# Kernel tuning notes

Hardware: AMD Instinct MI355X
Metric: run time of the kernel (lower is better)

The kernel has to match this reference:

```python
import jax, jax.numpy as jnp
import numpy as np

HIDDEN = 1024
HEADS = 16
HEAD = HIDDEN // HEADS
B, S = 2, 2048


def setup_inputs() -> dict:
    key = jax.random.key(0)
    ks = jax.random.split(key, 8)
    query = jax.random.normal(ks[0], (B, S, HIDDEN), dtype=jnp.float32)
    key_t = jax.random.normal(ks[1], (B, S, HIDDEN), dtype=jnp.float32)
    value = jax.random.normal(ks[2], (B, S, HIDDEN), dtype=jnp.float32)
    # causal mask, broadcastable over batch and heads; 0 -> masked (-inf)
    mask = jnp.tril(jnp.ones((S, S), dtype=jnp.int32))[None, None, :, :]
    # torch Linear weights are [out_features, in_features]
    scale = 0.02
    Wq = jax.random.normal(ks[3], (HIDDEN, HIDDEN), dtype=jnp.float32) * scale
    Wk = jax.random.normal(ks[4], (HIDDEN, HIDDEN), dtype=jnp.float32) * scale
    Wv = jax.random.normal(ks[5], (HIDDEN, HIDDEN), dtype=jnp.float32) * scale
    Wo = jax.random.normal(ks[6], (HIDDEN, HIDDEN), dtype=jnp.float32) * scale
    bo = jax.random.normal(ks[7], (HIDDEN,), dtype=jnp.float32) * scale
    return {"query": query, "key": key_t, "value": value, "mask": mask,
            "Wq": Wq, "Wk": Wk, "Wv": Wv, "Wo": Wo, "bo": bo}


def reference(query, key, value, mask, Wq, Wk, Wv, Wo, bo):
    b = query.shape[0]
    # Linear (no bias): x @ W^T, then split into heads -> [b, h, s, d]
    def heads(x, W):
        y = jnp.einsum('bse,oe->bso', x, W)
        return y.reshape(b, -1, HEADS, HEAD).transpose(0, 2, 1, 3)
    Q = heads(query, Wq)
    K = heads(key, Wk)
    V = heads(value, Wv)
    inv_scale = 1.0 / jnp.sqrt(jnp.float32(HEAD))
    scores = jnp.einsum('bhqd,bhkd->bhqk', Q, K) * inv_scale  # [b,h,s,s]
    scores = jnp.where(mask == 0, -jnp.inf, scores)
    attn = jax.nn.softmax(scores, axis=-1)
    x = jnp.einsum('bhqk,bhkd->bhqd', attn, V)
    x = x.transpose(0, 2, 1, 3).reshape(b, -1, HIDDEN)
    return jnp.einsum('bse,oe->bso', x, Wo) + bo
```

## Files before the change

kernel.cpp:

```cpp
#include <hip/hip_runtime.h>


typedef __attribute__((ext_vector_type(8))) short short8;
typedef __attribute__((ext_vector_type(4))) float f32x4;
typedef unsigned int u32;
typedef unsigned short u16;

__device__ inline f32x4 mfma16(short8 a, short8 b, f32x4 c) {
    return __builtin_amdgcn_mfma_f32_16x16x32_bf16(a, b, c, 0, 0, 0);
}
__device__ inline u16 f2bf(float f) {
    union { float f; u32 u; } v; v.f = f;
    u32 r = v.u + 0x7fff + ((v.u >> 16) & 1);
    return (u16)(r >> 16);
}
__device__ inline void gll16(void* lds, const void* g) {
    __builtin_amdgcn_global_load_lds((const __attribute__((address_space(1))) u32*)g,
                                     (__attribute__((address_space(3))) u32*)lds,
                                     16, 0, 0);
}
__device__ inline u32 pkbf(float hi, float lo) {
    return __builtin_amdgcn_perm(__float_as_uint(hi), __float_as_uint(lo),
                                 0x07060302u);
}

__global__ __launch_bounds__(256)
void cvt_all(const float* __restrict__ q, const float* __restrict__ k,
             const float* __restrict__ v, const float* __restrict__ wq,
             const float* __restrict__ wk, const float* __restrict__ wv,
             const float* __restrict__ wo,
             u16* __restrict__ q16, u16* __restrict__ k16,
             u16* __restrict__ v16, u16* __restrict__ w16) {
    const size_t QKV = 1u << 22;
    const size_t WSZ = 1u << 20;
    size_t base = ((size_t)blockIdx.x * 256 + threadIdx.x) * 8;
    const float* src; u16* dst; size_t off; float scale = 1.0f;
    if (base < QKV)            { src = q; dst = q16; off = base;
                                 scale = 0.125f * 1.44269504f; }
    else if (base < 2 * QKV)   { src = k; dst = k16; off = base - QKV;     }
    else if (base < 3 * QKV)   { src = v; dst = v16; off = base - 2 * QKV; }
    else {
        size_t wb = base - 3 * QKV;
        int wi = (int)(wb >> 20); off = wb & (WSZ - 1);
        src = wi == 0 ? wq : wi == 1 ? wk : wi == 2 ? wv : wo;
        dst = w16 + (size_t)wi * WSZ;
    }
    float4 f0 = *(const float4*)(src + off);
    float4 f1 = *(const float4*)(src + off + 4);
    short8 s = { (short)f2bf(f0.x * scale), (short)f2bf(f0.y * scale),
                 (short)f2bf(f0.z * scale), (short)f2bf(f0.w * scale),
                 (short)f2bf(f1.x * scale), (short)f2bf(f1.y * scale),
                 (short)f2bf(f1.z * scale), (short)f2bf(f1.w * scale) };
    *(short8*)(dst + off) = s;
}

__global__ __launch_bounds__(256)
void gemm_qkv(const u16* __restrict__ q16, const u16* __restrict__ k16,
              const u16* __restrict__ v16, const u16* __restrict__ w16,
              u16* __restrict__ Qg, u16* __restrict__ Kg, u16* __restrict__ Vt) {
    const int K = 1024;
    __shared__ u16 As[2][128 * 64];
    __shared__ u16 Bs[2][128 * 64];
    const int z = blockIdx.z;
    const u16* A = z == 0 ? q16 : z == 1 ? k16 : v16;
    const u16* W = w16 + (size_t)z * (1u << 20);

    const int tid = threadIdx.x, lane = tid & 63, w = tid >> 6;
    const int ln15 = lane & 15, quad = lane >> 4, s7 = ln15 & 7;
    const int lr = lane >> 3;
    const int lcs = (((lane & 7) ^ lr) << 3);
    const int m0 = blockIdx.y * 128, n0 = blockIdx.x * 128;
    const int wm = (w >> 1) * 64, wn = (w & 1) * 64;

    f32x4 acc[4][4] = {};

    #pragma unroll
    for (int c = 0; c < 4; ++c) {
        gll16(&As[0][(w * 32 + c * 8) * 64],
              &A[(size_t)(m0 + w * 32 + c * 8 + lr) * K + lcs]);
        gll16(&Bs[0][(w * 32 + c * 8) * 64],
              &W[(size_t)(n0 + w * 32 + c * 8 + lr) * K + lcs]);
    }

    for (int i = 0; i < 16; ++i) {
        const int cur = i & 1;
        if (i < 15) {
            const int nb = cur ^ 1, k0 = (i + 1) * 64;
            #pragma unroll
            for (int c = 0; c < 4; ++c) {
                gll16(&As[nb][(w * 32 + c * 8) * 64],
                      &A[(size_t)(m0 + w * 32 + c * 8 + lr) * K + k0 + lcs]);
                gll16(&Bs[nb][(w * 32 + c * 8) * 64],
                      &W[(size_t)(n0 + w * 32 + c * 8 + lr) * K + k0 + lcs]);
            }
            __asm__ volatile("s_waitcnt vmcnt(8)" ::: "memory");
        } else {
            __asm__ volatile("s_waitcnt vmcnt(0)" ::: "memory");
        }
        __builtin_amdgcn_s_barrier();

        #pragma unroll
        for (int kh = 0; kh < 2; ++kh) {
            short8 a[4], b[4];
            #pragma unroll
            for (int mt = 0; mt < 4; ++mt)
                a[mt] = *(const short8*)&As[cur][(wm + mt * 16 + ln15) * 64 +
                                                (((kh * 4 + quad) ^ s7) << 3)];
            #pragma unroll
            for (int nt = 0; nt < 4; ++nt)
                b[nt] = *(const short8*)&Bs[cur][(wn + nt * 16 + ln15) * 64 +
                                                (((kh * 4 + quad) ^ s7) << 3)];
            #pragma unroll
            for (int mt = 0; mt < 4; ++mt)
                #pragma unroll
                for (int nt = 0; nt < 4; ++nt)
                    acc[mt][nt] = mfma16(a[mt], b[nt], acc[mt][nt]);
        }
        __builtin_amdgcn_s_barrier();
    }

    #pragma unroll
    for (int mt = 0; mt < 4; ++mt)
        #pragma unroll
        for (int nt = 0; nt < 4; ++nt)
            #pragma unroll
            for (int r = 0; r < 4; ++r) {
                int m = m0 + wm + mt * 16 + quad * 4 + r;
                int n = n0 + wn + nt * 16 + ln15;
                u16 hv = f2bf(acc[mt][nt][r]);
                if (z == 2) {
                    int b_ = m >> 11, s_ = m & 2047, h_ = n >> 6, d_ = n & 63;
                    int kl = s_ & 63;
                    int sp = (s_ & ~63) + (kl & 15) * 4 + (kl >> 4);
                    Vt[((size_t)(b_ * 16 + h_) * 64 + d_) * 2048 + sp] = hv;
                } else {
                    u16* dst = z ? Kg : Qg;
                    dst[(size_t)m * 1024 + n] = hv;
                }
            }
}

__global__ __launch_bounds__(256)
void gemm_out(const u16* __restrict__ A, const u16* __restrict__ W,
              const float* __restrict__ bias, float* __restrict__ out) {
    const int K = 1024;
    __shared__ u16 As[2][64 * 64];
    __shared__ u16 Bs[2][128 * 64];
    const int id = blockIdx.x;
    const int by = id >> 3, bx = id & 7;

    const int tid = threadIdx.x, lane = tid & 63, w = tid >> 6;
    const int ln15 = lane & 15, quad = lane >> 4, s7 = ln15 & 7;
    const int lr = lane >> 3;
    const int lcs = (((lane & 7) ^ lr) << 3);
    const int m0 = by * 64, n0 = bx * 128;
    const int wm = (w & 1) * 32, wn = (w >> 1) * 64;

    f32x4 acc[2][4] = {};

    #pragma unroll
    for (int c = 0; c < 2; ++c)
        gll16(&As[0][(w * 16 + c * 8) * 64],
              &A[(size_t)(m0 + w * 16 + c * 8 + lr) * K + lcs]);
    #pragma unroll
    for (int c = 0; c < 4; ++c)
        gll16(&Bs[0][(w * 32 + c * 8) * 64],
              &W[(size_t)(n0 + w * 32 + c * 8 + lr) * K + lcs]);

    for (int i = 0; i < 16; ++i) {
        const int cur = i & 1;
        if (i < 15) {
            const int nb = cur ^ 1, k0 = (i + 1) * 64;
            #pragma unroll
            for (int c = 0; c < 2; ++c)
                gll16(&As[nb][(w * 16 + c * 8) * 64],
                      &A[(size_t)(m0 + w * 16 + c * 8 + lr) * K + k0 + lcs]);
            #pragma unroll
            for (int c = 0; c < 4; ++c)
                gll16(&Bs[nb][(w * 32 + c * 8) * 64],
                      &W[(size_t)(n0 + w * 32 + c * 8 + lr) * K + k0 + lcs]);
            __asm__ volatile("s_waitcnt vmcnt(6)" ::: "memory");
        } else {
            __asm__ volatile("s_waitcnt vmcnt(0)" ::: "memory");
        }
        __builtin_amdgcn_s_barrier();

        #pragma unroll
        for (int kh = 0; kh < 2; ++kh) {
            short8 a[2], b[4];
            #pragma unroll
            for (int mt = 0; mt < 2; ++mt)
                a[mt] = *(const short8*)&As[cur][(wm + mt * 16 + ln15) * 64 +
                                                (((kh * 4 + quad) ^ s7) << 3)];
            #pragma unroll
            for (int nt = 0; nt < 4; ++nt)
                b[nt] = *(const short8*)&Bs[cur][(wn + nt * 16 + ln15) * 64 +
                                                (((kh * 4 + quad) ^ s7) << 3)];
            #pragma unroll
            for (int mt = 0; mt < 2; ++mt)
                #pragma unroll
                for (int nt = 0; nt < 4; ++nt)
                    acc[mt][nt] = mfma16(a[mt], b[nt], acc[mt][nt]);
        }
        __builtin_amdgcn_s_barrier();
    }

    #pragma unroll
    for (int mt = 0; mt < 2; ++mt)
        #pragma unroll
        for (int nt = 0; nt < 4; ++nt)
            #pragma unroll
            for (int r = 0; r < 4; ++r) {
                int m = m0 + wm + mt * 16 + quad * 4 + r;
                int n = n0 + wn + nt * 16 + ln15;
                out[(size_t)m * 1024 + n] = acc[mt][nt][r] + bias[n];
            }
}

__global__ __launch_bounds__(256)
void attn3(const u16* __restrict__ Qg, const u16* __restrict__ Kg,
           const u16* __restrict__ Vt, u16* __restrict__ Xb) {
    __shared__ u16 Kl[2][64 * 64];
    __shared__ u16 Vl[2][64 * 64];
    __shared__ u16 Pl[4][16 * 72];

    const int id = blockIdx.x;
    const int bh = id & 31, qt = 31 - (id >> 5);
    const int b = bh >> 4, h = bh & 15;
    const int tid = threadIdx.x, lane = tid & 63, w = tid >> 6;
    const int ln15 = lane & 15, quad = lane >> 4, s7 = ln15 & 7;
    const int lr = lane >> 3;
    const int lcs = (((lane & 7) ^ lr) << 3);
    const u16* Kbase = Kg + (size_t)b * 2048 * 1024 + h * 64;
    const u16* Vbase = Vt + (size_t)bh * 64 * 2048;
    const float M0L = 8.65617025f;
    const int q0 = qt * 64;

    const u16* qrow = Qg + (size_t)(b * 2048 + q0 + w * 16 + ln15) * 1024 + h * 64;
    short8 aq0 = *(const short8*)(qrow + quad * 8);
    short8 aq1 = *(const short8*)(qrow + 32 + quad * 8);
    __asm__ volatile("s_waitcnt vmcnt(0)" ::: "memory");

    f32x4 o[4] = {};
    float lsum[4] = {0.f, 0.f, 0.f, 0.f};

    #pragma unroll
    for (int c = 0; c < 2; ++c) {
        const int r0 = w * 16 + c * 8;
        gll16(&Kl[0][r0 * 64], Kbase + (size_t)(r0 + lr) * 1024 + lcs);
        gll16(&Vl[0][r0 * 64], Vbase + (size_t)(r0 + lr) * 2048 + lcs);
    }

    for (int kt = 0; kt <= qt; ++kt) {
        const int cur = kt & 1;
        if (kt < qt) {
            const int nb = cur ^ 1, nk = (kt + 1) * 64;
            #pragma unroll
            for (int c = 0; c < 2; ++c) {
                const int r0 = w * 16 + c * 8;
                gll16(&Kl[nb][r0 * 64], Kbase + (size_t)(nk + r0 + lr) * 1024 + lcs);
                gll16(&Vl[nb][r0 * 64], Vbase + (size_t)(r0 + lr) * 2048 + nk + lcs);
            }
            __asm__ volatile("s_waitcnt vmcnt(4)" ::: "memory");
        } else {
            __asm__ volatile("s_waitcnt vmcnt(0)" ::: "memory");
        }
        __builtin_amdgcn_s_barrier();

        f32x4 sc[4];
        #pragma unroll
        for (int ct = 0; ct < 4; ++ct) {
            short8 b0 = *(const short8*)&Kl[cur][(ct * 16 + ln15) * 64 +
                                                ((quad ^ s7) << 3)];
            short8 b1 = *(const short8*)&Kl[cur][(ct * 16 + ln15) * 64 +
                                                (((4 + quad) ^ s7) << 3)];
            f32x4 c = {};
            c = mfma16(aq0, b0, c);
            c = mfma16(aq1, b1, c);
            sc[ct] = c;
        }

        const bool diag = (kt == qt);
        #pragma unroll
        for (int r = 0; r < 4; ++r) {
            float s0 = sc[0][r], s1 = sc[1][r], s2 = sc[2][r], s3 = sc[3][r];
            if (diag) {
                const int qq = w * 16 + quad * 4 + r;
                s0 = (ln15      <= qq) ? s0 : -1e30f;
                s1 = (16 + ln15 <= qq) ? s1 : -1e30f;
                s2 = (32 + ln15 <= qq) ? s2 : -1e30f;
                s3 = (48 + ln15 <= qq) ? s3 : -1e30f;
            }
            float p0 = __builtin_amdgcn_exp2f(s0 - M0L);
            float p1 = __builtin_amdgcn_exp2f(s1 - M0L);
            float p2 = __builtin_amdgcn_exp2f(s2 - M0L);
            float p3 = __builtin_amdgcn_exp2f(s3 - M0L);
            uint2 pw = make_uint2(pkbf(p1, p0), pkbf(p3, p2));
            *(uint2*)&Pl[w][(quad * 4 + r) * 72 + ln15 * 4] = pw;
            lsum[r] += (p0 + p1) + (p2 + p3);
        }

        __asm__ volatile("s_waitcnt lgkmcnt(0)" ::: "memory");
        short8 ap0 = *(const short8*)&Pl[w][ln15 * 72 + quad * 8];
        short8 ap1 = *(const short8*)&Pl[w][ln15 * 72 + 32 + quad * 8];

        #pragma unroll
        for (int dt = 0; dt < 4; ++dt) {
            short8 bv0 = *(const short8*)&Vl[cur][(dt * 16 + ln15) * 64 +
                                                 ((quad ^ s7) << 3)];
            short8 bv1 = *(const short8*)&Vl[cur][(dt * 16 + ln15) * 64 +
                                                 (((4 + quad) ^ s7) << 3)];
            o[dt] = mfma16(ap0, bv0, o[dt]);
            o[dt] = mfma16(ap1, bv1, o[dt]);
        }
        __builtin_amdgcn_s_barrier();
    }

    #pragma unroll
    for (int r = 0; r < 4; ++r) {
        float l = lsum[r];
        #pragma unroll
        for (int off = 1; off < 16; off <<= 1)
            l += __shfl_xor(l, off);
        lsum[r] = l;
    }
    #pragma unroll
    for (int dt = 0; dt < 4; ++dt)
        #pragma unroll
        for (int r = 0; r < 4; ++r) {
            int q = q0 + w * 16 + quad * 4 + r;
            Xb[(size_t)(b * 2048 + q) * 1024 + h * 64 + dt * 16 + ln15] =
                f2bf(o[dt][r] / lsum[r]);
        }
}

extern "C" void kernel_launch(void* const* d_in, const int* in_sizes, int n_in,
                              void* d_out, int out_size, void* d_ws, size_t ws_size,
                              hipStream_t stream) {
    const float* query = (const float*)d_in[0];
    const float* key   = (const float*)d_in[1];
    const float* value = (const float*)d_in[2];
    const float* Wq = (const float*)d_in[4];
    const float* Wk = (const float*)d_in[5];
    const float* Wv = (const float*)d_in[6];
    const float* Wo = (const float*)d_in[7];
    const float* bo = (const float*)d_in[8];
    float* out = (float*)d_out;

    u16* ws  = (u16*)d_ws;
    const size_t T = 1ull << 22;
    u16* q16 = ws;
    u16* k16 = ws + T;
    u16* v16 = ws + 2 * T;
    u16* w16 = ws + 3 * T;
    u16* Qg  = ws + 4 * T;
    u16* Kg  = ws + 5 * T;
    u16* Vt  = (u16*)d_out;
    u16* Xb  = q16;
    const size_t WSZ = 1ull << 20;

    cvt_all<<<8192, 256, 0, stream>>>(query, key, value, Wq, Wk, Wv, Wo,
                                      q16, k16, v16, w16);

    gemm_qkv<<<dim3(8, 32, 3), 256, 0, stream>>>(q16, k16, v16, w16, Qg, Kg, Vt);

    attn3<<<1024, 256, 0, stream>>>(Qg, Kg, Vt, Xb);

    gemm_out<<<512, 256, 0, stream>>>(Xb, w16 + 3 * WSZ, bo, out);
}
```

Baseline: 228.4 us.

## Enlarge QKV GEMM tiles to 256x256 with 512 threads and split B-tile prefetch

```diff
diff --git a/kernel.cpp b/kernel.cpp
--- a/kernel.cpp
+++ b/kernel.cpp
@@ -54,13 +54,13 @@
     *(short8*)(dst + off) = s;
 }
 
-__global__ __launch_bounds__(256)
+__global__ __launch_bounds__(512, 2)
 void gemm_qkv(const u16* __restrict__ q16, const u16* __restrict__ k16,
               const u16* __restrict__ v16, const u16* __restrict__ w16,
               u16* __restrict__ Qg, u16* __restrict__ Kg, u16* __restrict__ Vt) {
     const int K = 1024;
-    __shared__ u16 As[2][128 * 64];
-    __shared__ u16 Bs[2][128 * 64];
+    __shared__ u16 As[2][256 * 64];
+    __shared__ u16 Bs[2][256 * 64];
     const int z = blockIdx.z;
     const u16* A = z == 0 ? q16 : z == 1 ? k16 : v16;
     const u16* W = w16 + (size_t)z * (1u << 20);
@@ -69,58 +69,86 @@
     const int ln15 = lane & 15, quad = lane >> 4, s7 = ln15 & 7;
     const int lr = lane >> 3;
     const int lcs = (((lane & 7) ^ lr) << 3);
-    const int m0 = blockIdx.y * 128, n0 = blockIdx.x * 128;
-    const int wm = (w >> 1) * 64, wn = (w & 1) * 64;
-
-    f32x4 acc[4][4] = {};
-
-    #pragma unroll
-    for (int c = 0; c < 4; ++c) {
+    const int m0 = blockIdx.y * 256, n0 = blockIdx.x * 256;
+    const int wm = (w >> 2) * 128, wn = (w & 3) * 64;
+
+    f32x4 acc[8][4] = {};
+
+    #pragma unroll
+    for (int c = 0; c < 4; ++c)
         gll16(&As[0][(w * 32 + c * 8) * 64],
               &A[(size_t)(m0 + w * 32 + c * 8 + lr) * K + lcs]);
+    #pragma unroll
+    for (int c = 0; c < 4; ++c)
         gll16(&Bs[0][(w * 32 + c * 8) * 64],
               &W[(size_t)(n0 + w * 32 + c * 8 + lr) * K + lcs]);
-    }
-
-    for (int i = 0; i < 16; ++i) {
-        const int cur = i & 1;
-        if (i < 15) {
-            const int nb = cur ^ 1, k0 = (i + 1) * 64;
-            #pragma unroll
-            for (int c = 0; c < 4; ++c) {
+
+    for (int t = 0; t < 16; ++t) {
+        const int cur = t & 1, nb = cur ^ 1;
+        const int k0 = (t + 1) * 64;
+        if (t < 15) {
+            #pragma unroll
+            for (int c = 0; c < 4; ++c)
                 gll16(&As[nb][(w * 32 + c * 8) * 64],
                       &A[(size_t)(m0 + w * 32 + c * 8 + lr) * K + k0 + lcs]);
-                gll16(&Bs[nb][(w * 32 + c * 8) * 64],
-                      &W[(size_t)(n0 + w * 32 + c * 8 + lr) * K + k0 + lcs]);
-            }
-            __asm__ volatile("s_waitcnt vmcnt(8)" ::: "memory");
+            __asm__ volatile("s_waitcnt vmcnt(4)" ::: "memory");
         } else {
             __asm__ volatile("s_waitcnt vmcnt(0)" ::: "memory");
         }
         __builtin_amdgcn_s_barrier();
-
-        #pragma unroll
-        for (int kh = 0; kh < 2; ++kh) {
-            short8 a[4], b[4];
-            #pragma unroll
-            for (int mt = 0; mt < 4; ++mt)
+        __builtin_amdgcn_sched_barrier(0);
+
+        {
+            short8 a[8], b[4];
+            #pragma unroll
+            for (int mt = 0; mt < 8; ++mt)
                 a[mt] = *(const short8*)&As[cur][(wm + mt * 16 + ln15) * 64 +
-                                                (((kh * 4 + quad) ^ s7) << 3)];
+                                                ((quad ^ s7) << 3)];
             #pragma unroll
             for (int nt = 0; nt < 4; ++nt)
                 b[nt] = *(const short8*)&Bs[cur][(wn + nt * 16 + ln15) * 64 +
-                                                (((kh * 4 + quad) ^ s7) << 3)];
-            #pragma unroll
-            for (int mt = 0; mt < 4; ++mt)
+                                                ((quad ^ s7) << 3)];
+            __builtin_amdgcn_s_setprio(1);
+            #pragma unroll
+            for (int mt = 0; mt < 8; ++mt)
                 #pragma unroll
                 for (int nt = 0; nt < 4; ++nt)
                     acc[mt][nt] = mfma16(a[mt], b[nt], acc[mt][nt]);
-        }
-        __builtin_amdgcn_s_barrier();
-    }
-
-    #pragma unroll
-    for (int mt = 0; mt < 4; ++mt)
+            __builtin_amdgcn_s_setprio(0);
+        }
+        __builtin_amdgcn_s_barrier();
+        __builtin_amdgcn_sched_barrier(0);
+
+        if (t < 15) {
+            #pragma unroll
+            for (int c = 0; c < 4; ++c)
+                gll16(&Bs[nb][(w * 32 + c * 8) * 64],
+                      &W[(size_t)(n0 + w * 32 + c * 8 + lr) * K + k0 + lcs]);
+        }
+
+        {
+            short8 a[8], b[4];
+            #pragma unroll
+            for (int mt = 0; mt < 8; ++mt)
+                a[mt] = *(const short8*)&As[cur][(wm + mt * 16 + ln15) * 64 +
+                                                (((4 + quad) ^ s7) << 3)];
+            #pragma unroll
+            for (int nt = 0; nt < 4; ++nt)
+                b[nt] = *(const short8*)&Bs[cur][(wn + nt * 16 + ln15) * 64 +
+                                                (((4 + quad) ^ s7) << 3)];
+            __builtin_amdgcn_s_setprio(1);
+            #pragma unroll
+            for (int mt = 0; mt < 8; ++mt)
+                #pragma unroll
+                for (int nt = 0; nt < 4; ++nt)
+                    acc[mt][nt] = mfma16(a[mt], b[nt], acc[mt][nt]);
+            __builtin_amdgcn_s_setprio(0);
+        }
+        __builtin_amdgcn_s_barrier();
+    }
+
+    #pragma unroll
+    for (int mt = 0; mt < 8; ++mt)
         #pragma unroll
         for (int nt = 0; nt < 4; ++nt)
             #pragma unroll
@@ -184,6 +212,7 @@
             __asm__ volatile("s_waitcnt vmcnt(0)" ::: "memory");
         }
         __builtin_amdgcn_s_barrier();
+        __builtin_amdgcn_sched_barrier(0);
 
         #pragma unroll
         for (int kh = 0; kh < 2; ++kh) {
@@ -362,7 +391,7 @@
     cvt_all<<<8192, 256, 0, stream>>>(query, key, value, Wq, Wk, Wv, Wo,
                                       q16, k16, v16, w16);
 
-    gemm_qkv<<<dim3(8, 32, 3), 256, 0, stream>>>(q16, k16, v16, w16, Qg, Kg, Vt);
+    gemm_qkv<<<dim3(4, 16, 3), 512, 0, stream>>>(q16, k16, v16, w16, Qg, Kg, Vt);
 
     attn3<<<1024, 256, 0, stream>>>(Qg, Kg, Vt, Xb);
 
```

Measured after the change: 237.1 us. 1.04x slower.
